# Kernel tuning notes

Hardware: AMD Instinct MI355X
Metric: run time of the kernel (lower is better)

## Reference

```python
import jax, jax.numpy as jnp
import numpy as np

T, E, D = 16, 200000, 64      # num_tables, rows per table, emb_dim
B, L = 4096, 20               # batch size, fixed bag length
BOUND = 0.000316              # EMB_WEIGHT_UNIFORM_INIT_BOUND


def setup_inputs() -> dict:
    key = jax.random.key(0)
    k1, k2 = jax.random.split(key)
    # FBGEMM TBE layout: indices concatenated over tables then batch,
    # offsets[t*B + b] marks bag start for (table t, sample b).
    indices = jax.random.randint(k1, (T * B * L,), 0, E, dtype=jnp.int32)
    offsets = jnp.arange(T * B + 1, dtype=jnp.int32) * L
    weights = jax.random.uniform(k2, (T, E, D), minval=-BOUND, maxval=BOUND,
                                 dtype=jnp.float32)
    return {"indices": indices, "offsets": offsets, "weights": weights}


def reference(indices, offsets, weights):
    N = indices.shape[0]
    # bag id for every index position: seg in [0, T*B)
    seg = jnp.searchsorted(offsets, jnp.arange(N, dtype=offsets.dtype),
                           side="right") - 1
    table = seg // B                       # which table each index belongs to
    embs = weights[table, indices]         # [N, D] gather
    pooled = jax.ops.segment_sum(embs, seg, num_segments=T * B)  # [T*B, D]
    # [T, B, D] -> [B, T, D] -> [B, T*D]  (per-sample concat over tables)
    return pooled.reshape(T, B, D).transpose(1, 0, 2).reshape(B, T * D)
```

## Files before the change

### kernel.cpp

```cpp
#include <hip/hip_runtime.h>

constexpr int T = 16;
constexpr int E = 200000;
constexpr int D = 64;
constexpr int B = 4096;
constexpr int L = 20;

__global__ __launch_bounds__(256) void tbe_pooled_fwd(
    const int*   __restrict__ indices,
    const int*   __restrict__ offsets,
    const float* __restrict__ weights,
    float*       __restrict__ out)
{
    const int tid  = threadIdx.x;
    const int lane = tid & 63;
    const int wave = tid >> 6;
    const int sub  = lane >> 4;
    const int col  = lane & 15;

    const int bag = blockIdx.x * 16 + wave * 4 + sub;
    const int t   = bag >> 12;
    const int b   = bag & (B - 1);

    const int start = offsets[bag];
    const int end   = offsets[bag + 1];
    const int n     = end - start;

    const float* tbl = weights + (size_t)t * E * D;

    float4 acc = make_float4(0.f, 0.f, 0.f, 0.f);

    if (n == L) {
        int idx[L];
#pragma unroll
        for (int l = 0; l < L; ++l) idx[l] = indices[start + l];
#pragma unroll
        for (int l = 0; l < L; ++l) {
            const float4 v = *reinterpret_cast<const float4*>(
                tbl + (size_t)idx[l] * D + col * 4);
            acc.x += v.x; acc.y += v.y; acc.z += v.z; acc.w += v.w;
        }
    } else {
        for (int l = 0; l < n; ++l) {
            const int i = indices[start + l];
            const float4 v = *reinterpret_cast<const float4*>(
                tbl + (size_t)i * D + col * 4);
            acc.x += v.x; acc.y += v.y; acc.z += v.z; acc.w += v.w;
        }
    }

    float4* outp = reinterpret_cast<float4*>(
        out + (size_t)b * (T * D) + t * D + col * 4);
    *outp = acc;
}

extern "C" void kernel_launch(void* const* d_in, const int* in_sizes, int n_in,
                              void* d_out, int out_size, void* d_ws, size_t ws_size,
                              hipStream_t stream) {
    const int*   indices = (const int*)  d_in[0];
    const int*   offsets = (const int*)  d_in[1];
    const float* weights = (const float*)d_in[2];
    float*       out     = (float*)      d_out;

    const int num_bags = T * B;
    const int blocks   = num_bags / 16;

    tbe_pooled_fwd<<<blocks, 256, 0, stream>>>(indices, offsets, weights, out);
}
```

Before: 925.8 us.

## Map one wavefront per bag with scalar-uniform indices and per-lane float loads

Changes the work mapping from four bags per wavefront (16 lanes each, float4 loads) to one bag per wavefront where each of the 64 lanes loads one float. The bag id is made wave-uniform via readfirstlane, so offsets and indices can be fetched with scalar loads and row addresses use 32-bit math. This is meant to cut per-lane index loads and vector address arithmetic, at the cost of four times as many blocks and narrower per-lane memory transactions.

```diff
diff --git a/kernel.cpp b/kernel.cpp
--- a/kernel.cpp
+++ b/kernel.cpp
@@ -12,13 +12,10 @@
     const float* __restrict__ weights,
     float*       __restrict__ out)
 {
-    const int tid  = threadIdx.x;
-    const int lane = tid & 63;
-    const int wave = tid >> 6;
-    const int sub  = lane >> 4;
-    const int col  = lane & 15;
+    const int lane = threadIdx.x & 63;
+    const int wave = threadIdx.x >> 6;
 
-    const int bag = blockIdx.x * 16 + wave * 4 + sub;
+    const int bag = __builtin_amdgcn_readfirstlane(blockIdx.x * 4 + wave);
     const int t   = bag >> 12;
     const int b   = bag & (B - 1);
 
@@ -26,32 +23,26 @@
     const int end   = offsets[bag + 1];
     const int n     = end - start;
 
-    const float* tbl = weights + (size_t)t * E * D;
+    const float* tbl = weights + (size_t)t * (E * D);
 
-    float4 acc = make_float4(0.f, 0.f, 0.f, 0.f);
+    float acc = 0.f;
 
     if (n == L) {
         int idx[L];
 #pragma unroll
-        for (int l = 0; l < L; ++l) idx[l] = indices[start + l];
+        for (int l = 0; l < L; ++l)
+            idx[l] = indices[start + l];
 #pragma unroll
-        for (int l = 0; l < L; ++l) {
-            const float4 v = *reinterpret_cast<const float4*>(
-                tbl + (size_t)idx[l] * D + col * 4);
-            acc.x += v.x; acc.y += v.y; acc.z += v.z; acc.w += v.w;
-        }
+        for (int l = 0; l < L; ++l)
+            acc += tbl[(uint32_t)idx[l] * D + lane];
     } else {
         for (int l = 0; l < n; ++l) {
             const int i = indices[start + l];
-            const float4 v = *reinterpret_cast<const float4*>(
-                tbl + (size_t)i * D + col * 4);
-            acc.x += v.x; acc.y += v.y; acc.z += v.z; acc.w += v.w;
+            acc += tbl[(uint32_t)i * D + lane];
         }
     }
 
-    float4* outp = reinterpret_cast<float4*>(
-        out + (size_t)b * (T * D) + t * D + col * 4);
-    *outp = acc;
+    out[(size_t)b * (T * D) + t * D + lane] = acc;
 }
 
 extern "C" void kernel_launch(void* const* d_in, const int* in_sizes, int n_in,
@@ -63,7 +54,7 @@
     float*       out     = (float*)      d_out;
 
     const int num_bags = T * B;
-    const int blocks   = num_bags / 16;
+    const int blocks   = num_bags / 4;
 
     tbe_pooled_fwd<<<blocks, 256, 0, stream>>>(indices, offsets, weights, out);
 }
```

New measurement: 927.1 us. No clear change (+0.1%).
